# Optimization experiments

Measured on AMD Instinct MI355X. Metric: run time of the kernel, lower is better.

Reference implementation:

```python
import jax, jax.numpy as jnp
import numpy as np

D = 768
EXPAND = 4
D_INNER = EXPAND * D
G = 32
EPS = 1e-5


def setup_inputs() -> dict:
    key = jax.random.key(0)
    ks = jax.random.split(key, 10)
    B, T = 16, G * G
    s = lambda fan_in: 1.0 / np.sqrt(fan_in)
    return {
        "x": jax.random.normal(ks[0], (B, T, D), dtype=jnp.float32),
        "norm_w": jnp.ones((D,), dtype=jnp.float32),
        "w_proj": jax.random.normal(ks[1], (D_INNER, D), dtype=jnp.float32) * s(D),
        "w_gate": jax.random.normal(ks[2], (D_INNER, D), dtype=jnp.float32) * s(D),
        "conv_w": jax.random.normal(ks[3], (D_INNER, 1, 3, 3), dtype=jnp.float32) * s(9),
        "conv_b": jax.random.normal(ks[4], (D_INNER,), dtype=jnp.float32) * 0.01,
        "w_out": jax.random.normal(ks[5], (D, D_INNER), dtype=jnp.float32) * s(D_INNER),
        "w_k": jax.random.normal(ks[6], (D, D), dtype=jnp.float32) * s(D),
        "w_v": jax.random.normal(ks[7], (D, D), dtype=jnp.float32) * s(D),
        "log_alpha": jnp.array(0.0, dtype=jnp.float32),  # log(memory_alpha=1.0)
    }


def _rmsnorm(x, w):
    ms = jnp.mean(jnp.square(x.astype(jnp.float32)), axis=-1, keepdims=True)
    return x * jax.lax.rsqrt(ms + EPS).astype(x.dtype) * w


def reference(x, norm_w, w_proj, w_gate, conv_w, conv_b, w_out, w_k, w_v, log_alpha):
    B, T, _ = x.shape
    h = _rmsnorm(x, norm_w)                                   # [B,T,D]
    val = jnp.einsum("btd,ed->bte", h, w_proj)                # [B,T,dI]
    val = val.transpose(0, 2, 1).reshape(B, D_INNER, G, G)    # [B,dI,G,G]
    val = jax.lax.conv_general_dilated(
        val, conv_w, window_strides=(1, 1), padding=((1, 1), (1, 1)),
        dimension_numbers=("NCHW", "OIHW", "NCHW"),
        feature_group_count=D_INNER,
    ) + conv_b[None, :, None, None]
    val = jax.nn.silu(val)
    val = val.reshape(B, D_INNER, T).transpose(0, 2, 1)       # [B,T,dI]
    gated = val * jax.nn.silu(jnp.einsum("btd,ed->bte", h, w_gate))
    out = jnp.einsum("bte,de->btd", gated, w_out)             # [B,T,D]
    K = jnp.einsum("btd,ed->bte", h, w_k)                     # [B,T,D]
    V = jnp.einsum("btd,ed->bte", out, w_v)                   # [B,T,D]
    W = jnp.einsum("btd,bte->bde", K, V) / T                  # [B,D,D]
    read = jnp.einsum("btd,bde->bte", K, W)                   # [B,T,D]
    out = out + jnp.exp(log_alpha) * read
    return x + out
```

## Files before the change

kernel.cpp:

```cpp
#include <hip/hip_runtime.h>
#include <hip/hip_bf16.h>
#include <cstdint>
#include <cstddef>

typedef unsigned short u16;
typedef __attribute__((ext_vector_type(8))) __bf16 bf16x8;
typedef __attribute__((ext_vector_type(4))) float f32x4;
typedef __attribute__((ext_vector_type(8))) unsigned short us8;

#define NDM 768
#define NDI 3072
#define NTT 1024
#define NBB 16
#define NM (NBB*NTT)

__device__ __forceinline__ u16 f2bf(float f) {
  unsigned u = __builtin_bit_cast(unsigned, f);
  u += 0x7fffu + ((u >> 16) & 1u);
  return (u16)(u >> 16);
}
__device__ __forceinline__ float bf2f(u16 b) {
  return __builtin_bit_cast(float, ((unsigned)b) << 16);
}
__device__ __forceinline__ float silu_f(float v) {
  return v * (1.0f / (1.0f + __expf(-v)));
}
__device__ __forceinline__ void gload16(const u16* g, u16* l) {
  __builtin_amdgcn_global_load_lds((const __attribute__((address_space(1))) void*)g,
                                   (__attribute__((address_space(3))) void*)l, 16, 0, 0);
}

__global__ __launch_bounds__(256)
void k_f32_to_bf16(const float* __restrict__ in, u16* __restrict__ out, int n4) {
  const int i = blockIdx.x * 256 + threadIdx.x;
  if (i < n4) {
    float4 v = ((const float4*)in)[i];
    ushort4 o;
    o.x = f2bf(v.x); o.y = f2bf(v.y); o.z = f2bf(v.z); o.w = f2bf(v.w);
    ((ushort4*)out)[i] = o;
  }
}

__global__ __launch_bounds__(256)
void k_convw_t(const float* __restrict__ cw, u16* __restrict__ wTb) {
  const int e = blockIdx.x * 256 + threadIdx.x;
  if (e < NDI) {
#pragma unroll
    for (int t = 0; t < 9; t++) wTb[t * NDI + e] = f2bf(cw[e * 9 + t]);
  }
}

__global__ __launch_bounds__(256)
void k_rmsnorm(const float* __restrict__ x, const float* __restrict__ w, u16* __restrict__ h) {
  const int row  = blockIdx.x * 4 + (threadIdx.x >> 6);
  const int lane = threadIdx.x & 63;
  const float4* xr = (const float4*)(x + (size_t)row * NDM);
  float4 a = xr[lane], b = xr[lane + 64], c = xr[lane + 128];
  float ss = a.x*a.x + a.y*a.y + a.z*a.z + a.w*a.w
           + b.x*b.x + b.y*b.y + b.z*b.z + b.w*b.w
           + c.x*c.x + c.y*c.y + c.z*c.z + c.w*c.w;
#pragma unroll
  for (int off = 32; off > 0; off >>= 1) ss += __shfl_xor(ss, off);
  const float r = rsqrtf(ss * (1.0f / NDM) + 1e-5f);
  const float4* wr = (const float4*)w;
  float4 wa = wr[lane], wb = wr[lane + 64], wc = wr[lane + 128];
  ushort4 oa, ob, oc;
  oa.x = f2bf(a.x * r * wa.x); oa.y = f2bf(a.y * r * wa.y);
  oa.z = f2bf(a.z * r * wa.z); oa.w = f2bf(a.w * r * wa.w);
  ob.x = f2bf(b.x * r * wb.x); ob.y = f2bf(b.y * r * wb.y);
  ob.z = f2bf(b.z * r * wb.z); ob.w = f2bf(b.w * r * wb.w);
  oc.x = f2bf(c.x * r * wc.x); oc.y = f2bf(c.y * r * wc.y);
  oc.z = f2bf(c.z * r * wc.z); oc.w = f2bf(c.w * r * wc.w);
  ushort4* hr = (ushort4*)(h + (size_t)row * NDM);
  hr[lane] = oa; hr[lane + 64] = ob; hr[lane + 128] = oc;
}

template <int MODE>
__global__ __launch_bounds__(256)
void k_gemm_nt(const u16* __restrict__ A, const u16* __restrict__ B,
               void* __restrict__ C0, void* __restrict__ C1,
               const float* __restrict__ X, const float* __restrict__ scalep,
               int N, int Kd, int nTiles,
               long sAb, long sBb, long sCb, int mPerBatchB, long sBm) {
  __shared__ u16 smem[128 * 136];
  u16* As = smem;
  u16* Bs = smem + 4096;
  const int bz = blockIdx.z;
  A += (size_t)bz * sAb;
  B += (size_t)bz * sBb;

  const int nwg = gridDim.x;
  const int id = blockIdx.x;
  const int sid = ((nwg & 7) == 0) ? ((id & 7) * (nwg >> 3) + (id >> 3)) : id;
  const int mt = sid / nTiles, nt = sid - mt * nTiles;
  const int m0 = mt * 128, n0 = nt * 128;
  if (mPerBatchB > 0) B += (size_t)(m0 / mPerBatchB) * sBm;

  const int lane = threadIdx.x & 63, wid = threadIdx.x >> 6;
  const int wm = wid >> 1, wn = wid & 1;

  f32x4 zero = {0.f, 0.f, 0.f, 0.f};
  f32x4 acc[4][4];
#pragma unroll
  for (int m = 0; m < 4; m++)
#pragma unroll
    for (int n = 0; n < 4; n++) acc[m][n] = zero;

  const int kslot = ((lane & 3) ^ ((lane >> 3) & 3)) * 8;
  const u16* Ag = A + (size_t)(m0 + wid * 32 + (lane >> 2)) * Kd + kslot;
  const u16* Bg = B + (size_t)(n0 + wid * 32 + (lane >> 2)) * Kd + kslot;
  u16* AsW = &As[(wid * 32) * 32];
  u16* BsW = &Bs[(wid * 32) * 32];
  const int rowSkip = 16 * Kd;
  const int fr = lane & 15;
  const int xko = (((lane >> 4) ^ ((fr >> 1) & 3)) << 3);

  for (int kt = 0; kt < Kd; kt += 32) {
    gload16(Ag, AsW);
    gload16(Ag + rowSkip, AsW + 16 * 32);
    gload16(Bg, BsW);
    gload16(Bg + rowSkip, BsW + 16 * 32);
    Ag += 32; Bg += 32;
    __syncthreads();
    bf16x8 af[4], bfr[4];
#pragma unroll
    for (int m = 0; m < 4; m++)
      af[m] = *(const bf16x8*)&As[(wm * 64 + m * 16 + fr) * 32 + xko];
#pragma unroll
    for (int n = 0; n < 4; n++)
      bfr[n] = *(const bf16x8*)&Bs[(wn * 64 + n * 16 + fr) * 32 + xko];
#pragma unroll
    for (int m = 0; m < 4; m++)
#pragma unroll
      for (int n = 0; n < 4; n++)
        acc[m][n] = __builtin_amdgcn_mfma_f32_16x16x32_bf16(af[m], bfr[n], acc[m][n], 0, 0, 0);
    __syncthreads();
  }

  const size_t cb = (size_t)bz * sCb;

  if (MODE == 3) {
#pragma unroll
    for (int m = 0; m < 4; m++) {
#pragma unroll
      for (int n = 0; n < 4; n++) {
        const int col = n0 + wn * 64 + n * 16 + (lane & 15);
        const int rb  = m0 + wm * 64 + m * 16 + ((lane >> 4) << 2);
#pragma unroll
        for (int q = 0; q < 4; q++) {
          const size_t idx = (size_t)(rb + q) * N + col;
          ((float*)C0)[idx] = X[idx] + bf2f(((const u16*)C1)[idx]) + acc[m][n][q];
        }
      }
    }
    return;
  }

  float sc = 1.0f;
  if (MODE == 2) sc = __expf(scalep[0]) * (1.0f / 1024.0f);
#pragma unroll
  for (int m = 0; m < 4; m++) {
#pragma unroll
    for (int n = 0; n < 4; n++) {
      const int lc = wn * 64 + n * 16 + (lane & 15);
      const int lr = wm * 64 + m * 16 + ((lane >> 4) << 2);
#pragma unroll
      for (int q = 0; q < 4; q++) {
        const float v = acc[m][n][q];
        u16 o;
        if (MODE == 5) o = (n0 < 3072) ? f2bf(v) : f2bf(silu_f(v));
        else if (MODE == 2) o = f2bf(v * sc);
        else o = f2bf(v);
        smem[(lr + q) * 136 + lc] = o;
      }
    }
  }
  __syncthreads();

  u16* Cp;
  size_t base;
  int strideN;
  if (MODE == 5) {
    Cp = (n0 < 3072) ? (u16*)C0 : (u16*)C1;
    strideN = 3072;
    base = (size_t)m0 * 3072 + (size_t)((n0 < 3072) ? n0 : n0 - 3072);
  } else {
    Cp = (u16*)C0;
    strideN = N;
    base = cb + (size_t)m0 * N + n0;
  }
  const int t = threadIdx.x;
  const int seg = t & 15, rr = t >> 4;
#pragma unroll
  for (int p = 0; p < 8; p++) {
    const int r = p * 16 + rr;
    us8 v = *(const us8*)&smem[r * 136 + seg * 8];
    *(us8*)&Cp[base + (size_t)r * strideN + seg * 8] = v;
  }
}

__global__ __launch_bounds__(384)
void k_conv_gate(const u16* __restrict__ val, u16* __restrict__ gate,
                 const u16* __restrict__ wTb, const float* __restrict__ bias) {
  const int tid = threadIdx.x;
  const int m = blockIdx.x * 2 + (tid >= 192);
  const int e0 = (tid % 192) * 16;
  const int j = m & 31, i = (m >> 5) & 31;
  float acc[16];
  {
    const float4* bp = (const float4*)(bias + e0);
    float4 b0 = bp[0], b1 = bp[1], b2 = bp[2], b3 = bp[3];
    acc[0]=b0.x; acc[1]=b0.y; acc[2]=b0.z; acc[3]=b0.w;
    acc[4]=b1.x; acc[5]=b1.y; acc[6]=b1.z; acc[7]=b1.w;
    acc[8]=b2.x; acc[9]=b2.y; acc[10]=b2.z; acc[11]=b2.w;
    acc[12]=b3.x; acc[13]=b3.y; acc[14]=b3.z; acc[15]=b3.w;
  }
  const u16* vb = val + (size_t)m * NDI + e0;
#pragma unroll
  for (int di = -1; di <= 1; di++) {
    if ((unsigned)(i + di) >= 32u) continue;
#pragma unroll
    for (int dj = -1; dj <= 1; dj++) {
      if ((unsigned)(j + dj) >= 32u) continue;
      const u16* vp = vb + (ptrdiff_t)(di * 32 + dj) * NDI;
      us8 v0 = *(const us8*)vp, v1 = *(const us8*)(vp + 8);
      const u16* wp = wTb + ((di + 1) * 3 + (dj + 1)) * NDI + e0;
      us8 w0 = *(const us8*)wp, w1 = *(const us8*)(wp + 8);
#pragma unroll
      for (int q = 0; q < 8; q++) acc[q]     += bf2f(v0[q]) * bf2f(w0[q]);
#pragma unroll
      for (int q = 0; q < 8; q++) acc[8 + q] += bf2f(v1[q]) * bf2f(w1[q]);
    }
  }
  u16* gp = gate + (size_t)m * NDI + e0;
  us8 g0 = *(const us8*)gp, g1 = *(const us8*)(gp + 8);
  us8 o0, o1;
#pragma unroll
  for (int q = 0; q < 8; q++) o0[q] = f2bf(silu_f(acc[q]) * bf2f(g0[q]));
#pragma unroll
  for (int q = 0; q < 8; q++) o1[q] = f2bf(silu_f(acc[8 + q]) * bf2f(g1[q]));
  *(us8*)gp = o0;
  *(us8*)(gp + 8) = o1;
}

__global__ __launch_bounds__(256)
void k_transpose(const u16* __restrict__ in, u16* __restrict__ out) {
  __shared__ u16 tile[64][65];
  const int d0 = blockIdx.x * 64, t0 = blockIdx.y * 64, b = blockIdx.z;
  const int lx = threadIdx.x & 15, ly = threadIdx.x >> 4;
  const u16* ip = in + ((size_t)b * NTT + t0) * NDM + d0;
#pragma unroll
  for (int p = 0; p < 4; p++) {
    const int r = ly + p * 16;
    ushort4 v = *(const ushort4*)(ip + (size_t)r * NDM + lx * 4);
    tile[r][lx * 4 + 0] = v.x; tile[r][lx * 4 + 1] = v.y;
    tile[r][lx * 4 + 2] = v.z; tile[r][lx * 4 + 3] = v.w;
  }
  __syncthreads();
  u16* op = out + ((size_t)b * NDM + d0) * NTT + t0;
#pragma unroll
  for (int p = 0; p < 4; p++) {
    const int r = ly + p * 16;
    ushort4 v;
    v.x = tile[lx * 4 + 0][r]; v.y = tile[lx * 4 + 1][r];
    v.z = tile[lx * 4 + 2][r]; v.w = tile[lx * 4 + 3][r];
    *(ushort4*)(op + (size_t)r * NTT + lx * 4) = v;
  }
}

extern "C" void kernel_launch(void* const* d_in, const int* in_sizes, int n_in,
                              void* d_out, int out_size, void* d_ws, size_t ws_size,
                              hipStream_t stream) {
  const float* x      = (const float*)d_in[0];
  const float* norm_w = (const float*)d_in[1];
  const float* w_proj = (const float*)d_in[2];
  const float* w_gate = (const float*)d_in[3];
  const float* conv_w = (const float*)d_in[4];
  const float* conv_b = (const float*)d_in[5];
  const float* w_out  = (const float*)d_in[6];
  const float* w_k    = (const float*)d_in[7];
  const float* w_v    = (const float*)d_in[8];
  const float* lalpha = (const float*)d_in[9];

  char* ob = (char*)d_out;
  u16* h    = (u16*)(ob);
  u16* wcat = (u16*)(ob + 25165824);
  u16* wob  = (u16*)(ob + 34603008);
  u16* wkb  = (u16*)(ob + 39321600);
  u16* wvb  = (u16*)(ob + 40501248);
  u16* wTb  = (u16*)(ob + 41680896);

  char* ws = (char*)d_ws;
  u16* valp  = (u16*)(ws);
  u16* gateb = (u16*)(ws + 100663296);
  u16* outb  = (u16*)(ws);
  u16* Kbf   = (u16*)(ws + 25165824);
  u16* Vbf   = (u16*)(ws + 50331648);
  u16* Kt    = (u16*)(ws + 100663296);
  u16* Vt    = (u16*)(ws + 125829120);
  u16* Wt    = (u16*)(ws + 150994944);

  k_f32_to_bf16<<<2304, 256, 0, stream>>>(w_proj, wcat,           589824);
  k_f32_to_bf16<<<2304, 256, 0, stream>>>(w_gate, wcat + 2359296, 589824);
  k_f32_to_bf16<<<2304, 256, 0, stream>>>(w_out,  wob, 589824);
  k_f32_to_bf16<<<576,  256, 0, stream>>>(w_k,    wkb, 147456);
  k_f32_to_bf16<<<576,  256, 0, stream>>>(w_v,    wvb, 147456);
  k_convw_t<<<12, 256, 0, stream>>>(conv_w, wTb);

  k_rmsnorm<<<4096, 256, 0, stream>>>(x, norm_w, h);

  k_gemm_nt<5><<<6144, 256, 0, stream>>>(h, wcat, valp, gateb, nullptr, nullptr,
                                         6144, NDM, 48, 0, 0, 0, 0, 0);
  k_conv_gate<<<8192, 384, 0, stream>>>(valp, gateb, wTb, conv_b);

  k_gemm_nt<0><<<768, 256, 0, stream>>>(gateb, wob, outb, nullptr, nullptr, nullptr,
                                        NDM, NDI, 6, 0, 0, 0, 0, 0);
  k_gemm_nt<0><<<768, 256, 0, stream>>>(h, wkb, Kbf, nullptr, nullptr, nullptr,
                                        NDM, NDM, 6, 0, 0, 0, 0, 0);
  k_gemm_nt<0><<<768, 256, 0, stream>>>(outb, wvb, Vbf, nullptr, nullptr, nullptr,
                                        NDM, NDM, 6, 0, 0, 0, 0, 0);
  k_transpose<<<dim3(12, 16, 16), 256, 0, stream>>>(Kbf, Kt);
  k_transpose<<<dim3(12, 16, 16), 256, 0, stream>>>(Vbf, Vt);

  k_gemm_nt<2><<<dim3(36, 1, 16), 256, 0, stream>>>(Vt, Kt, Wt, nullptr, nullptr, lalpha,
                                                    NDM, NTT, 6,
                                                    (long)NDM * NTT, (long)NDM * NTT,
                                                    (long)NDM * NDM, 0, 0);
  k_gemm_nt<3><<<768, 256, 0, stream>>>(Kbf, Wt, d_out, outb, x, nullptr,
                                        NDM, NDM, 6, 0, 0, 0,
                                        NTT, (long)NDM * NDM);
}
```

Baseline: 753.5 us.

## Add 256x256-tile 8-wave double-buffered GEMM for fused proj/gate projection

```diff
diff --git a/kernel.cpp b/kernel.cpp
--- a/kernel.cpp
+++ b/kernel.cpp
@@ -75,6 +75,100 @@
   hr[lane] = oa; hr[lane + 64] = ob; hr[lane + 128] = oc;
 }
 
+__device__ __forceinline__ void stage8(const u16* Asrc, const u16* Bsrc, u16* smem,
+                                       int cur, int wid) {
+  u16* Ad = smem + cur * 16384 + wid * 512;
+  u16* Bd = smem + 32768 + cur * 16384 + wid * 512;
+#pragma unroll
+  for (int i = 0; i < 4; i++) {
+    gload16(Asrc + i * 49152, Ad + i * 4096);
+    gload16(Bsrc + i * 49152, Bd + i * 4096);
+  }
+}
+
+__global__ __launch_bounds__(512, 2)
+void k_gemm8p(const u16* __restrict__ A, const u16* __restrict__ B,
+              u16* __restrict__ Cv, u16* __restrict__ Cg) {
+  __shared__ u16 smem[65536];
+  const int nwg = gridDim.x;
+  const int id = blockIdx.x;
+  const int sid = ((nwg & 7) == 0) ? ((id & 7) * (nwg >> 3) + (id >> 3)) : id;
+  const int mt = sid / 24, ntile = sid - mt * 24;
+  const int m0 = mt * 256, n0 = ntile * 256;
+
+  const int tid = threadIdx.x;
+  const int lane = tid & 63, wid = tid >> 6;
+  const int wm = wid >> 2, wn = wid & 3;
+  const int fr = lane & 15, l4 = lane >> 4;
+
+  const int srow = tid >> 3;
+  const int sslot = (tid & 7) ^ (srow & 7);
+  const u16* Asrc = A + (size_t)(m0 + srow) * 768 + sslot * 8;
+  const u16* Bsrc = B + (size_t)(n0 + srow) * 768 + sslot * 8;
+
+  f32x4 acc[8][4];
+#pragma unroll
+  for (int m = 0; m < 8; m++)
+#pragma unroll
+    for (int n = 0; n < 4; n++) acc[m][n] = (f32x4){0.f, 0.f, 0.f, 0.f};
+
+  stage8(Asrc,      Bsrc,      smem, 0, wid);
+  stage8(Asrc + 64, Bsrc + 64, smem, 1, wid);
+
+  int cur = 0;
+#pragma unroll 1
+  for (int t = 0; t < 12; t++) {
+    if (t == 11) asm volatile("s_waitcnt vmcnt(0)" ::: "memory");
+    else         asm volatile("s_waitcnt vmcnt(8)" ::: "memory");
+    __builtin_amdgcn_s_barrier();
+
+    const u16* Abuf = smem + cur * 16384;
+    const u16* Bbuf = smem + 32768 + cur * 16384;
+
+    bf16x8 bfrag[4][2];
+#pragma unroll
+    for (int nf = 0; nf < 4; nf++) {
+      const int brow = wn * 64 + nf * 16 + fr;
+#pragma unroll
+      for (int s = 0; s < 2; s++)
+        bfrag[nf][s] = *(const bf16x8*)&Bbuf[brow * 64 + (((s << 2) + l4) ^ (brow & 7)) * 8];
+    }
+#pragma unroll
+    for (int mf = 0; mf < 8; mf++) {
+      const int arow = wm * 128 + mf * 16 + fr;
+      bf16x8 a0 = *(const bf16x8*)&Abuf[arow * 64 + ((l4)     ^ (arow & 7)) * 8];
+      bf16x8 a1 = *(const bf16x8*)&Abuf[arow * 64 + ((4 + l4) ^ (arow & 7)) * 8];
+#pragma unroll
+      for (int nf = 0; nf < 4; nf++) {
+        acc[mf][nf] = __builtin_amdgcn_mfma_f32_16x16x32_bf16(a0, bfrag[nf][0], acc[mf][nf], 0, 0, 0);
+        acc[mf][nf] = __builtin_amdgcn_mfma_f32_16x16x32_bf16(a1, bfrag[nf][1], acc[mf][nf], 0, 0, 0);
+      }
+    }
+    asm volatile("s_waitcnt lgkmcnt(0)" ::: "memory");
+    __builtin_amdgcn_s_barrier();
+    if (t < 10) stage8(Asrc + (t + 2) * 64, Bsrc + (t + 2) * 64, smem, cur, wid);
+    cur ^= 1;
+  }
+
+  const bool gate = (n0 >= 3072);
+  u16* Cp = gate ? Cg : Cv;
+  const int cb = gate ? n0 - 3072 : n0;
+#pragma unroll
+  for (int mf = 0; mf < 8; mf++) {
+#pragma unroll
+    for (int nf = 0; nf < 4; nf++) {
+      const int col = cb + wn * 64 + nf * 16 + fr;
+      const int rb  = m0 + wm * 128 + mf * 16 + (l4 << 2);
+#pragma unroll
+      for (int q = 0; q < 4; q++) {
+        float v = acc[mf][nf][q];
+        if (gate) v = silu_f(v);
+        Cp[(size_t)(rb + q) * 3072 + col] = f2bf(v);
+      }
+    }
+  }
+}
+
 template <int MODE>
 __global__ __launch_bounds__(256)
 void k_gemm_nt(const u16* __restrict__ A, const u16* __restrict__ B,
@@ -167,35 +261,21 @@
 #pragma unroll
       for (int q = 0; q < 4; q++) {
         const float v = acc[m][n][q];
-        u16 o;
-        if (MODE == 5) o = (n0 < 3072) ? f2bf(v) : f2bf(silu_f(v));
-        else if (MODE == 2) o = f2bf(v * sc);
-        else o = f2bf(v);
-        smem[(lr + q) * 136 + lc] = o;
+        smem[(lr + q) * 136 + lc] = (MODE == 2) ? f2bf(v * sc) : f2bf(v);
       }
     }
   }
   __syncthreads();
 
-  u16* Cp;
-  size_t base;
-  int strideN;
-  if (MODE == 5) {
-    Cp = (n0 < 3072) ? (u16*)C0 : (u16*)C1;
-    strideN = 3072;
-    base = (size_t)m0 * 3072 + (size_t)((n0 < 3072) ? n0 : n0 - 3072);
-  } else {
-    Cp = (u16*)C0;
-    strideN = N;
-    base = cb + (size_t)m0 * N + n0;
-  }
+  u16* Cp = (u16*)C0;
+  const size_t base = cb + (size_t)m0 * N + n0;
   const int t = threadIdx.x;
   const int seg = t & 15, rr = t >> 4;
 #pragma unroll
   for (int p = 0; p < 8; p++) {
     const int r = p * 16 + rr;
     us8 v = *(const us8*)&smem[r * 136 + seg * 8];
-    *(us8*)&Cp[base + (size_t)r * strideN + seg * 8] = v;
+    *(us8*)&Cp[base + (size_t)r * N + seg * 8] = v;
   }
 }
 
@@ -309,8 +389,8 @@
 
   k_rmsnorm<<<4096, 256, 0, stream>>>(x, norm_w, h);
 
-  k_gemm_nt<5><<<6144, 256, 0, stream>>>(h, wcat, valp, gateb, nullptr, nullptr,
-                                         6144, NDM, 48, 0, 0, 0, 0, 0);
+  k_gemm8p<<<1536, 512, 0, stream>>>(h, wcat, valp, gateb);
+
   k_conv_gate<<<8192, 384, 0, stream>>>(valp, gateb, wTb, conv_b);
 
   k_gemm_nt<0><<<768, 256, 0, stream>>>(gateb, wob, outb, nullptr, nullptr, nullptr,
```

Result: faster. 706.5 us (-6.2%).
